# Performance work log

Measured on AMD Instinct MI355X. Metric: run time of the kernel, lower is better.

The kernel has to match this reference:

```python
import jax, jax.numpy as jnp
import numpy as np

H = 512      # hidden_dim
K = 3        # conv_kernel_size
CHUNK = 3    # chunk_size
EPS = 1e-5   # BatchNorm eps


def conv1d(x, w, b, pad):
    # x: (B, Cin, L), w: (Cout, Cin, K)
    y = jax.lax.conv_general_dilated(x, w, (1,), [(pad, pad)],
                                     dimension_numbers=("NCH", "OIH", "NCH"))
    return y + b[None, :, None]


def chunk_indices(seq_lens):
    # static int metadata -> numpy index build (loop over small fixed batch only)
    sl = np.asarray(seq_lens)
    bidx, sidx = [], []
    for b, l in enumerate(sl):
        starts = np.arange(0, int(l) - CHUNK + 1, CHUNK)
        bidx.append(np.full(starts.shape[0], b, dtype=np.int32))
        sidx.append(starts.astype(np.int32))
    return np.concatenate(bidx), np.concatenate(sidx)


def setup_inputs() -> dict:
    key = jax.random.key(0)
    ks = jax.random.split(key, 8)
    B, L = 32, 4096
    x = jax.random.normal(ks[0], (B, L), jnp.float32)
    seq_lens = jax.random.randint(ks[1], (B,), 2048, L + 1)

    def w(k, shape):
        return jax.random.normal(k, shape, jnp.float32) * 0.05

    return {
        "x": x,
        "w0": w(ks[2], (H, 1, K)), "b0": jnp.zeros((H,)), "g0": jnp.ones((H,)), "be0": jnp.zeros((H,)),
        "w1": w(ks[3], (H, H, K)), "b1": jnp.zeros((H,)), "g1": jnp.ones((H,)), "be1": jnp.zeros((H,)),
        "w2": w(ks[4], (H, H, K)), "b2": jnp.zeros((H,)), "g2": jnp.ones((H,)), "be2": jnp.zeros((H,)),
        "pw": w(ks[5], (H, H, CHUNK)), "pb": jnp.zeros((H,)),
        "fw": w(ks[6], (1, H)), "fb": jnp.zeros((1,)),
        "seq_lens": seq_lens,
    }


def reference(x, w0, b0, g0, be0, w1, b1, g1, be1, w2, b2, g2, be2,
              pw, pb, fw, fb, seq_lens):
    inv = np.float32(1.0 / np.sqrt(1.0 + EPS))  # BN eval: mean=0, var=1
    h = x[:, None, :]  # (B, 1, L)
    for (w, b, g, be) in ((w0, b0, g0, be0), (w1, b1, g1, be1), (w2, b2, g2, be2)):
        h = jax.nn.relu(conv1d(h, w, b, pad=1))
        h = (g * inv)[None, :, None] * h + be[None, :, None]
    h = jnp.transpose(h, (0, 2, 1))  # (B, L, H)

    bidx_np, sidx_np = chunk_indices(seq_lens)
    bidx = jnp.asarray(bidx_np)
    sidx = jnp.asarray(sidx_np)
    offs = jnp.arange(CHUNK, dtype=jnp.int32)
    chunks = h[bidx[:, None], sidx[:, None] + offs[None, :], :]  # (N, CHUNK, H)

    # pre_fc_conv over a length-CHUNK window == one GEMM per chunk
    z = jnp.einsum("nth,cht->nc", chunks, pw) + pb  # (N, H)
    logits = jax.nn.relu(z) @ fw.T + fb             # (N, 1)
    return jax.nn.sigmoid(logits)[:, 0]             # (N,)
```

## Files before the change

kernel.cpp:

```cpp
#include <hip/hip_runtime.h>

#define HCH 512
#define LSEQ 4096
#define NB 32
#define KW 3
#define KDIM 1536
#define SPAD 1408
#define INVS 0.9999950000374997f
#define NT 24

typedef __attribute__((ext_vector_type(8))) short bf16x8;
typedef __attribute__((ext_vector_type(4))) float f32x4;

__device__ inline unsigned short f2bf(float f) {
  unsigned int u = __float_as_uint(f);
  u += 0x7fffu + ((u >> 16) & 1u);
  return (unsigned short)(u >> 16);
}

__device__ inline void gl_lds16(const void* g, void* l) {
  __builtin_amdgcn_global_load_lds(
      (const __attribute__((address_space(1))) void*)g,
      (__attribute__((address_space(3))) void*)l, 16, 0, 0);
}

__global__ void prep_all(const float* __restrict__ w1, const float* __restrict__ w2,
                         const float* __restrict__ pw, unsigned short* __restrict__ wt,
                         const int* __restrict__ seq_lens, int* __restrict__ cum,
                         float* __restrict__ pz, int nz) {
  int idx = blockIdx.x * 256 + threadIdx.x;
  if (idx < nz) pz[idx] = 0.f;
  if (idx == 0) {
    int acc = 0;
    for (int b = 0; b < NB; b++) {
      cum[b] = acc;
      acc += (seq_lens[b] - KW) / KW + 1;
    }
  }
  if (idx < 3 * HCH * KDIM) {
    int which = idx / (HCH * KDIM);
    int r = idx % (HCH * KDIM);
    int c = r / KDIM;
    int rem = r % KDIM;
    int k = rem / HCH, ci = rem % HCH;
    const float* src = (which == 0) ? w1 : ((which == 1) ? w2 : pw);
    wt[idx] = f2bf(src[c * KDIM + ci * KW + k]);
  }
}

__global__ void layer0(const float* __restrict__ x, const float* __restrict__ w0,
                       const float* __restrict__ b0, const float* __restrict__ g0,
                       const float* __restrict__ be0, unsigned short* __restrict__ h0,
                       const int* __restrict__ seq_q) {
  int tid = threadIdx.x;
  int wave = tid >> 6, lane = tid & 63;
  int pos0 = (blockIdx.x * 4 + wave) * 8;
  int l0 = pos0 & (LSEQ - 1);
  if (l0 >= seq_q[pos0 >> 12] + 2) return;
  int c0 = lane * 8;

  float w[24], bb[8], gg[8], ee[8];
  for (int v = 0; v < 6; v++)
    *reinterpret_cast<float4*>(w + v * 4) = *reinterpret_cast<const float4*>(w0 + c0 * 3 + v * 4);
  for (int v = 0; v < 2; v++) {
    *reinterpret_cast<float4*>(bb + v * 4) = *reinterpret_cast<const float4*>(b0 + c0 + v * 4);
    *reinterpret_cast<float4*>(gg + v * 4) = *reinterpret_cast<const float4*>(g0 + c0 + v * 4);
    *reinterpret_cast<float4*>(ee + v * 4) = *reinterpret_cast<const float4*>(be0 + c0 + v * 4);
  }
  for (int c = 0; c < 8; c++) gg[c] *= INVS;

  const float* xb = x + (size_t)(pos0 - l0);
  for (int pp = 0; pp < 8; pp++) {
    int l = l0 + pp;
    float xm1 = (l > 0) ? xb[l - 1] : 0.f;
    float xc = xb[l];
    float xp1 = (l < LSEQ - 1) ? xb[l + 1] : 0.f;
    unsigned int o[4];
    for (int pq = 0; pq < 4; pq++) {
      unsigned int lo = 0, hi = 0;
      for (int s = 0; s < 2; s++) {
        int c = pq * 2 + s;
        float y = w[c * 3] * xm1 + w[c * 3 + 1] * xc + w[c * 3 + 2] * xp1 + bb[c];
        y = fmaxf(y, 0.f);
        unsigned int u = f2bf(gg[c] * y + ee[c]);
        if (s == 0) lo = u; else hi = u;
      }
      o[pq] = lo | (hi << 16);
    }
    uint4 v4; v4.x = o[0]; v4.y = o[1]; v4.z = o[2]; v4.w = o[3];
    *reinterpret_cast<uint4*>(h0 + (size_t)(pos0 + pp) * HCH + c0) = v4;
  }
}

#define STAGE_A(Mh, nbuf, tn)                                               \
  { char* d_ = ldsc + ((nbuf)*4 + (Mh)) * 16384 + w * 1024;                 \
    gl_lds16(aSrc[Mh][0] + (tn)*64, d_);                                    \
    gl_lds16(aSrc[Mh][1] + (tn)*64, d_ + 8192); }

#define STAGE_B(Nh, nbuf, tn)                                               \
  { int k_ = (tn) >> 3, ci0_ = ((tn) & 7) << 6;                             \
    int p0_ = bRow[Nh][0] + k_, p1_ = bRow[Nh][1] + k_;                     \
    const unsigned short* s0_ = ((unsigned)p0_ < 4096u)                     \
        ? hin + hb + (size_t)p0_ * HCH + ci0_ + sslot8 : zp + sslot8;       \
    const unsigned short* s1_ = ((unsigned)p1_ < 4096u)                     \
        ? hin + hb + (size_t)p1_ * HCH + ci0_ + sslot8 : zp + sslot8;       \
    char* d_ = ldsc + ((nbuf)*4 + 2 + (Nh)) * 16384 + w * 1024;             \
    gl_lds16(s0_, d_); gl_lds16(s1_, d_ + 8192); }

#define LOAD_AF(Mh, buf)                                                    \
  _Pragma("unroll") for (int i_ = 0; i_ < 4; ++i_)                          \
  _Pragma("unroll") for (int s_ = 0; s_ < 2; ++s_)                          \
    af[i_][s_] = *reinterpret_cast<const bf16x8*>(                          \
        ldsb + ((buf)*4 + (Mh)) * 8192 + (wm + i_*16 + mr) * 64 +           \
        (((s_*4 + quad) ^ (mr & 7)) << 3));

#define LOAD_BF(Nh, buf)                                                    \
  _Pragma("unroll") for (int j_ = 0; j_ < 2; ++j_)                          \
  _Pragma("unroll") for (int s_ = 0; s_ < 2; ++s_)                          \
    bfv[Nh][j_][s_] = *reinterpret_cast<const bf16x8*>(                     \
        ldsb + ((buf)*4 + 2 + (Nh)) * 8192 + (wn + j_*16 + mr) * 64 +       \
        (((s_*4 + quad) ^ (mr & 7)) << 3));

#define MFMA_Q(Mh, Nh)                                                      \
  __builtin_amdgcn_s_setprio(1);                                            \
  _Pragma("unroll") for (int i_ = 0; i_ < 4; ++i_)                          \
  _Pragma("unroll") for (int j_ = 0; j_ < 2; ++j_)                          \
  _Pragma("unroll") for (int s_ = 0; s_ < 2; ++s_)                          \
    acc[(Mh)*4 + i_][(Nh)*2 + j_] = __builtin_amdgcn_mfma_f32_16x16x32_bf16( \
        af[i_][s_], bfv[Nh][j_][s_], acc[(Mh)*4 + i_][(Nh)*2 + j_], 0, 0, 0); \
  __builtin_amdgcn_s_setprio(0);

#define BARRIER { asm volatile("" ::: "memory");                            \
                  __builtin_amdgcn_s_barrier();                             \
                  asm volatile("" ::: "memory"); }
#define WAITV(n) asm volatile("s_waitcnt vmcnt(" #n ")" ::: "memory");

__global__ __launch_bounds__(512, 2) void conv_gemm8(
    const unsigned short* __restrict__ hin,
    const unsigned short* __restrict__ wT,
    const float* __restrict__ bconv, const float* __restrict__ g,
    const float* __restrict__ be,
    unsigned short* __restrict__ hout,
    const unsigned short* __restrict__ zp,
    const int* __restrict__ seq_q, int margin) {
  __shared__ unsigned short ldsb[8 * 8192];

  int f = blockIdx.x;
  int cpx = gridDim.x >> 3;
  int s = (f & 7) * cpx + (f >> 3);
  int cm = (s & 1) << 8;
  int y = s >> 1;
  int b = y >> 4;
  int l0 = (y & 15) << 8;
  int limit = seq_q[b] + margin;
  if (l0 >= limit) return;

  const size_t hb = (size_t)b * LSEQ * HCH;
  int tid = threadIdx.x;
  int w = tid >> 6, lane = tid & 63;
  int quad = lane >> 4, mr = lane & 15;
  int wm = (w >> 2) << 6;
  int wn = (w & 3) << 5;
  int srow = tid >> 3;
  int sslot8 = (((tid & 7) ^ (srow & 7)) << 3);

  const unsigned short* aSrc[2][2];
#pragma unroll
  for (int Mh = 0; Mh < 2; ++Mh)
#pragma unroll
    for (int g2 = 0; g2 < 2; ++g2)
      aSrc[Mh][g2] = wT + (size_t)(cm + Mh*128 + g2*64 + srow) * KDIM + sslot8;
  int bRow[2][2];
#pragma unroll
  for (int Nh = 0; Nh < 2; ++Nh)
#pragma unroll
    for (int g2 = 0; g2 < 2; ++g2)
      bRow[Nh][g2] = l0 - 1 + Nh*128 + g2*64 + srow;

  f32x4 acc[8][4] = {};
  char* ldsc = (char*)ldsb;

  STAGE_A(0, 0, 0); STAGE_A(1, 0, 0); STAGE_B(0, 0, 0); STAGE_B(1, 0, 0);

#pragma unroll 2
  for (int t = 0; t < NT; ++t) {
    int buf = t & 1, nbuf = buf ^ 1;
    int tn = (t + 1 < NT) ? t + 1 : t;
    bf16x8 af[4][2], bfv[2][2][2];
    WAITV(4);
    BARRIER;
    STAGE_A(0, nbuf, tn); STAGE_A(1, nbuf, tn);
    STAGE_B(0, nbuf, tn); STAGE_B(1, nbuf, tn);
    LOAD_AF(0, buf);
    WAITV(8);
    LOAD_BF(0, buf); LOAD_BF(1, buf);
    MFMA_Q(0, 0);
    MFMA_Q(0, 1);
    LOAD_AF(1, buf);
    MFMA_Q(1, 1);
    MFMA_Q(1, 0);
  }

#pragma unroll
  for (int ai = 0; ai < 8; ++ai) {
    int Mh = ai >> 2, i = ai & 3;
    int c = cm + Mh*128 + wm + i*16 + quad*4;
    f32x4 bc = *reinterpret_cast<const f32x4*>(bconv + c);
    f32x4 gg = *reinterpret_cast<const f32x4*>(g + c);
    f32x4 bb = *reinterpret_cast<const f32x4*>(be + c);
#pragma unroll
    for (int aj = 0; aj < 4; ++aj) {
      int Nh = aj >> 1, j = aj & 1;
      int n = l0 + Nh*128 + wn + j*16 + (lane & 15);
      if (n >= limit) continue;
      unsigned long long pack = 0;
#pragma unroll
      for (int r = 0; r < 4; ++r) {
        float yv = acc[ai][aj][r] + bc[r];
        yv = fmaxf(yv, 0.f);
        unsigned long long u = f2bf(gg[r] * INVS * yv + bb[r]);
        pack |= u << (16 * r);
      }
      *reinterpret_cast<unsigned long long*>(hout + hb + (size_t)n * HCH + c) = pack;
    }
  }
}

__global__ __launch_bounds__(256) void chunk_gemm(
    const unsigned short* __restrict__ h2,
    const unsigned short* __restrict__ wTp,
    const float* __restrict__ pb, const float* __restrict__ fw,
    const int* __restrict__ seq_q,
    const int* __restrict__ cum_q,
    float* __restrict__ partial,
    const unsigned short* __restrict__ zp) {
  __shared__ unsigned short As[3 * 128 * 32];
  __shared__ unsigned short Bs[384 * 32];

  int tid = threadIdx.x;
  int wave = tid >> 6, lane = tid & 63;
  int cm = blockIdx.x * 128;
  int b = blockIdx.y / (SPAD / 128);
  int s_base = (blockIdx.y % (SPAD / 128)) * 128;
  int slen = seq_q[b];
  if (3 * s_base + KW > slen) return;
  int p_base = 3 * s_base;
  int wm = (wave >> 1) * 64;
  int wn = (wave & 1) * 64;
  const size_t hb = (size_t)b * LSEQ * HCH;

  f32x4 acc[4][4] = {};

  int lr = lane >> 2, lc = (lane & 3) * 8;

  const unsigned short* bptr[6];
  const unsigned short* aptr[6];
  unsigned aoff[6];
  for (int t = 0; t < 6; t++) {
    int c = wave * 6 + t;
    int p = p_base + c * 16 + lr;
    bptr[t] = (p < LSEQ) ? (h2 + hb + (size_t)p * HCH + lc) : (zp + lc);
    int k = c >> 3, c8 = c & 7;
    aptr[t] = wTp + (size_t)(cm + c8 * 16 + lr) * KDIM + k * HCH + lc;
    aoff[t] = (unsigned)(k * 4096 + c8 * 512) * 2;
  }

  for (int it = 0; it < 16; it++) {
    int ci0 = it * 32;
    for (int t = 0; t < 6; t++) {
      gl_lds16(aptr[t] + ci0, (char*)As + aoff[t]);
      gl_lds16(bptr[t] + ci0, (char*)Bs + (wave * 6 + t) * 1024);
    }
    __syncthreads();

    int quad = lane >> 4, mr = lane & 15;
    for (int t = 0; t < 3; t++) {
      bf16x8 af[4], bfr[4];
      for (int i = 0; i < 4; i++)
        af[i] = *reinterpret_cast<const bf16x8*>(As + t * 4096 + (wm + i * 16 + mr) * 32 + quad * 8);
      for (int j = 0; j < 4; j++)
        bfr[j] = *reinterpret_cast<const bf16x8*>(Bs + (3 * (wn + j * 16 + mr) + t) * 32 + quad * 8);
      for (int i = 0; i < 4; i++)
        for (int j = 0; j < 4; j++)
          acc[i][j] = __builtin_amdgcn_mfma_f32_16x16x32_bf16(af[i], bfr[j], acc[i][j], 0, 0, 0);
    }
    __syncthreads();
  }

  int quad = lane >> 4, nn = lane & 15;
  for (int j = 0; j < 4; j++) {
    float s = 0.f;
    for (int i = 0; i < 4; i++) {
      int c = cm + wm + i * 16 + quad * 4;
      f32x4 pbv = *reinterpret_cast<const f32x4*>(pb + c);
      f32x4 fwv = *reinterpret_cast<const f32x4*>(fw + c);
      for (int r = 0; r < 4; r++) {
        float z = acc[i][j][r] + pbv[r];
        z = fmaxf(z, 0.f);
        s += z * fwv[r];
      }
    }
    s += __shfl_xor(s, 16, 64);
    s += __shfl_xor(s, 32, 64);
    if (quad == 0) {
      int sc = s_base + wn + j * 16 + nn;
      if (3 * sc + KW <= slen) atomicAdd(partial + cum_q[b] + sc, s);
    }
  }
}

__global__ void finalize(const float* __restrict__ partial, const float* __restrict__ fb,
                         float* __restrict__ out, int n) {
  int i = blockIdx.x * 256 + threadIdx.x;
  if (i < n) {
    float t = partial[i] + fb[0];
    out[i] = 1.f / (1.f + expf(-t));
  }
}

extern "C" void kernel_launch(void* const* d_in, const int* in_sizes, int n_in,
                              void* d_out, int out_size, void* d_ws, size_t ws_size,
                              hipStream_t stream) {
  (void)in_sizes; (void)n_in;
  const float* x   = (const float*)d_in[0];
  const float* w0  = (const float*)d_in[1];
  const float* b0  = (const float*)d_in[2];
  const float* g0  = (const float*)d_in[3];
  const float* be0 = (const float*)d_in[4];
  const float* w1  = (const float*)d_in[5];
  const float* b1  = (const float*)d_in[6];
  const float* g1  = (const float*)d_in[7];
  const float* be1 = (const float*)d_in[8];
  const float* w2  = (const float*)d_in[9];
  const float* b2  = (const float*)d_in[10];
  const float* g2  = (const float*)d_in[11];
  const float* be2 = (const float*)d_in[12];
  const float* pw  = (const float*)d_in[13];
  const float* pb  = (const float*)d_in[14];
  const float* fw  = (const float*)d_in[15];
  const float* fb  = (const float*)d_in[16];
  const int* seq_lens = (const int*)d_in[17];

  char* ws = (char*)d_ws;
  unsigned short* zeropage = (unsigned short*)ws;
  float* partial = (float*)(ws + 4096);
  size_t off = 4096 + (size_t)out_size * 4;
  off = (off + 255) & ~(size_t)255;
  int* cum = (int*)(ws + off);
  off += NB * 4;
  off = (off + 255) & ~(size_t)255;
  unsigned short* wt = (unsigned short*)(ws + off);
  off += (size_t)3 * HCH * KDIM * 2;
  off = (off + 255) & ~(size_t)255;
  size_t fixed = off;

  const size_t per_batch = (size_t)LSEQ * HCH * 2;
  int nb_pass = NB;
  while (nb_pass > 1 && fixed + 2 * per_batch * (size_t)nb_pass > ws_size)
    nb_pass >>= 1;
  unsigned short* h0 = (unsigned short*)(ws + fixed);
  unsigned short* h1 = h0 + (size_t)nb_pass * LSEQ * HCH;

  int nzero = 1024 + out_size;
  prep_all<<<(3 * HCH * KDIM) / 256, 256, 0, stream>>>(w1, w2, pw, wt, seq_lens, cum,
                                                       (float*)ws, nzero);

  int npass = NB / nb_pass;
  for (int q = 0; q < npass; q++) {
    const float* xq = x + (size_t)q * nb_pass * LSEQ;
    const int* sq = seq_lens + q * nb_pass;
    int nwg = nb_pass * 32;
    layer0<<<nb_pass * (LSEQ / 32), 256, 0, stream>>>(xq, w0, b0, g0, be0, h0, sq);
    conv_gemm8<<<nwg, 512, 0, stream>>>(h0, wt, b1, g1, be1, h1, zeropage, sq, 1);
    conv_gemm8<<<nwg, 512, 0, stream>>>(h1, wt + (size_t)HCH * KDIM, b2, g2, be2, h0,
                                        zeropage, sq, 0);
    chunk_gemm<<<dim3(4, nb_pass * (SPAD / 128)), 256, 0, stream>>>(
        h0, wt + (size_t)2 * HCH * KDIM, pb, fw,
        sq, cum + q * nb_pass, partial, zeropage);
  }
  finalize<<<(out_size + 255) / 256, 256, 0, stream>>>(partial, fb, (float*)d_out, out_size);
}
```

Baseline: 614.4 us.

## Pad activation buffers with zero rows and deepen B prefetch pipeline in conv GEMM

Activation buffers get a zeroed halo row on each side of every sequence (stride LSEQ+4), which removes the per-load bounds check and zero-page redirection for the conv B operand. The conv GEMM main loop is fully unrolled into 24 steps with A double-buffered and B triple-buffered, so B loads are issued two steps ahead. The K loop order is also changed to interleave the three taps. LDS use rises to 160KB per block, which may limit occupancy to one block per CU despite launch_bounds(512,2).

```diff
diff --git a/kernel.cpp b/kernel.cpp
--- a/kernel.cpp
+++ b/kernel.cpp
@@ -2,6 +2,7 @@
 
 #define HCH 512
 #define LSEQ 4096
+#define HSTR (LSEQ + 4)
 #define NB 32
 #define KW 3
 #define KDIM 1536
@@ -27,7 +28,8 @@
 __global__ void prep_all(const float* __restrict__ w1, const float* __restrict__ w2,
                          const float* __restrict__ pw, unsigned short* __restrict__ wt,
                          const int* __restrict__ seq_lens, int* __restrict__ cum,
-                         float* __restrict__ pz, int nz) {
+                         float* __restrict__ pz, int nz,
+                         unsigned short* __restrict__ hbuf, int nbp) {
   int idx = blockIdx.x * 256 + threadIdx.x;
   if (idx < nz) pz[idx] = 0.f;
   if (idx == 0) {
@@ -36,6 +38,15 @@
       cum[b] = acc;
       acc += (seq_lens[b] - KW) / KW + 1;
     }
+  }
+  int npads = 2 * nbp * 4 * HCH;
+  if (idx < npads) {
+    int per = nbp * 4 * HCH;
+    int buf = idx / per, r = idx % per;
+    int b = r / (4 * HCH), rr = r % (4 * HCH);
+    int j = rr / HCH, c = rr % HCH;
+    int row = (j == 0) ? 0 : (LSEQ + j);
+    hbuf[((size_t)buf * nbp + b) * HSTR * HCH + (size_t)row * HCH + c] = 0;
   }
   if (idx < 3 * HCH * KDIM) {
     int which = idx / (HCH * KDIM);
@@ -56,7 +67,8 @@
   int wave = tid >> 6, lane = tid & 63;
   int pos0 = (blockIdx.x * 4 + wave) * 8;
   int l0 = pos0 & (LSEQ - 1);
-  if (l0 >= seq_q[pos0 >> 12] + 2) return;
+  int bq = pos0 >> 12;
+  if (l0 >= seq_q[bq] + 2) return;
   int c0 = lane * 8;
 
   float w[24], bb[8], gg[8], ee[8];
@@ -70,6 +82,7 @@
   for (int c = 0; c < 8; c++) gg[c] *= INVS;
 
   const float* xb = x + (size_t)(pos0 - l0);
+  unsigned short* hrow = h0 + ((size_t)bq * HSTR + 1 + l0) * HCH + c0;
   for (int pp = 0; pp < 8; pp++) {
     int l = l0 + pp;
     float xm1 = (l > 0) ? xb[l - 1] : 0.f;
@@ -88,38 +101,35 @@
       o[pq] = lo | (hi << 16);
     }
     uint4 v4; v4.x = o[0]; v4.y = o[1]; v4.z = o[2]; v4.w = o[3];
-    *reinterpret_cast<uint4*>(h0 + (size_t)(pos0 + pp) * HCH + c0) = v4;
-  }
-}
-
-#define STAGE_A(Mh, nbuf, tn)                                               \
-  { char* d_ = ldsc + ((nbuf)*4 + (Mh)) * 16384 + w * 1024;                 \
-    gl_lds16(aSrc[Mh][0] + (tn)*64, d_);                                    \
-    gl_lds16(aSrc[Mh][1] + (tn)*64, d_ + 8192); }
-
-#define STAGE_B(Nh, nbuf, tn)                                               \
-  { int k_ = (tn) >> 3, ci0_ = ((tn) & 7) << 6;                             \
-    int p0_ = bRow[Nh][0] + k_, p1_ = bRow[Nh][1] + k_;                     \
-    const unsigned short* s0_ = ((unsigned)p0_ < 4096u)                     \
-        ? hin + hb + (size_t)p0_ * HCH + ci0_ + sslot8 : zp + sslot8;       \
-    const unsigned short* s1_ = ((unsigned)p1_ < 4096u)                     \
-        ? hin + hb + (size_t)p1_ * HCH + ci0_ + sslot8 : zp + sslot8;       \
-    char* d_ = ldsc + ((nbuf)*4 + 2 + (Nh)) * 16384 + w * 1024;             \
-    gl_lds16(s0_, d_); gl_lds16(s1_, d_ + 8192); }
-
-#define LOAD_AF(Mh, buf)                                                    \
+    *reinterpret_cast<uint4*>(hrow + (size_t)pp * HCH) = v4;
+  }
+}
+
+#define OFFK(T) (((T) % 3) * HCH + ((T) / 3) * 64)
+
+#define STAGE_A(Mh, AB, TN)                                                 \
+  { char* d_ = ldsc + (AB) * 32768 + (Mh) * 16384 + w * 1024;               \
+    gl_lds16(aSrc[Mh][0] + OFFK(TN), d_);                                   \
+    gl_lds16(aSrc[Mh][1] + OFFK(TN), d_ + 8192); }
+
+#define STAGE_B(Nh, BB, TN)                                                 \
+  { char* d_ = ldsc + 65536 + (BB) * 32768 + (Nh) * 16384 + w * 1024;       \
+    gl_lds16(bSrc[Nh][0] + OFFK(TN), d_);                                   \
+    gl_lds16(bSrc[Nh][1] + OFFK(TN), d_ + 8192); }
+
+#define LOAD_AF(Mh, AB)                                                     \
   _Pragma("unroll") for (int i_ = 0; i_ < 4; ++i_)                          \
   _Pragma("unroll") for (int s_ = 0; s_ < 2; ++s_)                          \
     af[i_][s_] = *reinterpret_cast<const bf16x8*>(                          \
-        ldsb + ((buf)*4 + (Mh)) * 8192 + (wm + i_*16 + mr) * 64 +           \
-        (((s_*4 + quad) ^ (mr & 7)) << 3));
-
-#define LOAD_BF(Nh, buf)                                                    \
+        ldsb + (AB) * 16384 + (Mh) * 8192 + (wm + i_ * 16 + mr) * 64 +      \
+        (((s_ * 4 + quad) ^ (mr & 7)) << 3));
+
+#define LOAD_BF(Nh, BB)                                                     \
   _Pragma("unroll") for (int j_ = 0; j_ < 2; ++j_)                          \
   _Pragma("unroll") for (int s_ = 0; s_ < 2; ++s_)                          \
     bfv[Nh][j_][s_] = *reinterpret_cast<const bf16x8*>(                     \
-        ldsb + ((buf)*4 + 2 + (Nh)) * 8192 + (wn + j_*16 + mr) * 64 +       \
-        (((s_*4 + quad) ^ (mr & 7)) << 3));
+        ldsb + 32768 + (BB) * 16384 + (Nh) * 8192 + (wn + j_ * 16 + mr) * 64 + \
+        (((s_ * 4 + quad) ^ (mr & 7)) << 3));
 
 #define MFMA_Q(Mh, Nh)                                                      \
   __builtin_amdgcn_s_setprio(1);                                            \
@@ -135,15 +145,30 @@
                   asm volatile("" ::: "memory"); }
 #define WAITV(n) asm volatile("s_waitcnt vmcnt(" #n ")" ::: "memory");
 
+#define STEP(T)                                                             \
+  {                                                                         \
+    if ((T) == NT - 1) { WAITV(0); } else { WAITV(4); }                     \
+    BARRIER;                                                                \
+    if ((T) + 1 < NT) { STAGE_A(0, ((T)+1)&1, (T)+1);                       \
+                        STAGE_A(1, ((T)+1)&1, (T)+1); }                     \
+    if ((T) + 2 < NT) { STAGE_B(0, ((T)+2)%3, (T)+2);                       \
+                        STAGE_B(1, ((T)+2)%3, (T)+2); }                     \
+    bf16x8 af[4][2], bfv[2][2][2];                                          \
+    LOAD_AF(0, (T)&1);                                                      \
+    LOAD_BF(0, (T)%3); LOAD_BF(1, (T)%3);                                   \
+    MFMA_Q(0, 0); MFMA_Q(0, 1);                                             \
+    LOAD_AF(1, (T)&1);                                                      \
+    MFMA_Q(1, 1); MFMA_Q(1, 0);                                             \
+  }
+
 __global__ __launch_bounds__(512, 2) void conv_gemm8(
     const unsigned short* __restrict__ hin,
     const unsigned short* __restrict__ wT,
     const float* __restrict__ bconv, const float* __restrict__ g,
     const float* __restrict__ be,
     unsigned short* __restrict__ hout,
-    const unsigned short* __restrict__ zp,
     const int* __restrict__ seq_q, int margin) {
-  __shared__ unsigned short ldsb[8 * 8192];
+  __shared__ unsigned short ldsb[81920];
 
   int f = blockIdx.x;
   int cpx = gridDim.x >> 3;
@@ -155,7 +180,7 @@
   int limit = seq_q[b] + margin;
   if (l0 >= limit) return;
 
-  const size_t hb = (size_t)b * LSEQ * HCH;
+  const size_t hb = (size_t)b * HSTR * HCH + HCH;
   int tid = threadIdx.x;
   int w = tid >> 6, lane = tid & 63;
   int quad = lane >> 4, mr = lane & 15;
@@ -169,49 +194,38 @@
   for (int Mh = 0; Mh < 2; ++Mh)
 #pragma unroll
     for (int g2 = 0; g2 < 2; ++g2)
-      aSrc[Mh][g2] = wT + (size_t)(cm + Mh*128 + g2*64 + srow) * KDIM + sslot8;
-  int bRow[2][2];
+      aSrc[Mh][g2] = wT + (size_t)(cm + Mh * 128 + g2 * 64 + srow) * KDIM + sslot8;
+  const unsigned short* bSrc[2][2];
 #pragma unroll
   for (int Nh = 0; Nh < 2; ++Nh)
 #pragma unroll
     for (int g2 = 0; g2 < 2; ++g2)
-      bRow[Nh][g2] = l0 - 1 + Nh*128 + g2*64 + srow;
+      bSrc[Nh][g2] = hin + hb +
+          (size_t)(l0 - 1 + Nh * 128 + g2 * 64 + srow) * HCH + sslot8;
 
   f32x4 acc[8][4] = {};
   char* ldsc = (char*)ldsb;
 
-  STAGE_A(0, 0, 0); STAGE_A(1, 0, 0); STAGE_B(0, 0, 0); STAGE_B(1, 0, 0);
-
-#pragma unroll 2
-  for (int t = 0; t < NT; ++t) {
-    int buf = t & 1, nbuf = buf ^ 1;
-    int tn = (t + 1 < NT) ? t + 1 : t;
-    bf16x8 af[4][2], bfv[2][2][2];
-    WAITV(4);
-    BARRIER;
-    STAGE_A(0, nbuf, tn); STAGE_A(1, nbuf, tn);
-    STAGE_B(0, nbuf, tn); STAGE_B(1, nbuf, tn);
-    LOAD_AF(0, buf);
-    WAITV(8);
-    LOAD_BF(0, buf); LOAD_BF(1, buf);
-    MFMA_Q(0, 0);
-    MFMA_Q(0, 1);
-    LOAD_AF(1, buf);
-    MFMA_Q(1, 1);
-    MFMA_Q(1, 0);
-  }
+  STAGE_A(0, 0, 0); STAGE_A(1, 0, 0);
+  STAGE_B(0, 0, 0); STAGE_B(1, 0, 0);
+  STAGE_B(0, 1, 1); STAGE_B(1, 1, 1);
+
+  STEP(0)  STEP(1)  STEP(2)  STEP(3)  STEP(4)  STEP(5)
+  STEP(6)  STEP(7)  STEP(8)  STEP(9)  STEP(10) STEP(11)
+  STEP(12) STEP(13) STEP(14) STEP(15) STEP(16) STEP(17)
+  STEP(18) STEP(19) STEP(20) STEP(21) STEP(22) STEP(23)
 
 #pragma unroll
   for (int ai = 0; ai < 8; ++ai) {
     int Mh = ai >> 2, i = ai & 3;
-    int c = cm + Mh*128 + wm + i*16 + quad*4;
+    int c = cm + Mh * 128 + wm + i * 16 + quad * 4;
     f32x4 bc = *reinterpret_cast<const f32x4*>(bconv + c);
     f32x4 gg = *reinterpret_cast<const f32x4*>(g + c);
     f32x4 bb = *reinterpret_cast<const f32x4*>(be + c);
 #pragma unroll
     for (int aj = 0; aj < 4; ++aj) {
       int Nh = aj >> 1, j = aj & 1;
-      int n = l0 + Nh*128 + wn + j*16 + (lane & 15);
+      int n = l0 + Nh * 128 + wn + j * 16 + (lane & 15);
       if (n >= limit) continue;
       unsigned long long pack = 0;
 #pragma unroll
@@ -247,7 +261,7 @@
   int p_base = 3 * s_base;
   int wm = (wave >> 1) * 64;
   int wn = (wave & 1) * 64;
-  const size_t hb = (size_t)b * LSEQ * HCH;
+  const size_t hb = (size_t)b * HSTR * HCH + HCH;
 
   f32x4 acc[4][4] = {};
 
@@ -354,16 +368,16 @@
   off = (off + 255) & ~(size_t)255;
   size_t fixed = off;
 
-  const size_t per_batch = (size_t)LSEQ * HCH * 2;
+  const size_t per_batch = (size_t)HSTR * HCH * 2;
   int nb_pass = NB;
   while (nb_pass > 1 && fixed + 2 * per_batch * (size_t)nb_pass > ws_size)
     nb_pass >>= 1;
   unsigned short* h0 = (unsigned short*)(ws + fixed);
-  unsigned short* h1 = h0 + (size_t)nb_pass * LSEQ * HCH;
+  unsigned short* h1 = h0 + (size_t)nb_pass * HSTR * HCH;
 
   int nzero = 1024 + out_size;
   prep_all<<<(3 * HCH * KDIM) / 256, 256, 0, stream>>>(w1, w2, pw, wt, seq_lens, cum,
-                                                       (float*)ws, nzero);
+                                                       (float*)ws, nzero, h0, nb_pass);
 
   int npass = NB / nb_pass;
   for (int q = 0; q < npass; q++) {
@@ -371,9 +385,9 @@
     const int* sq = seq_lens + q * nb_pass;
     int nwg = nb_pass * 32;
     layer0<<<nb_pass * (LSEQ / 32), 256, 0, stream>>>(xq, w0, b0, g0, be0, h0, sq);
-    conv_gemm8<<<nwg, 512, 0, stream>>>(h0, wt, b1, g1, be1, h1, zeropage, sq, 1);
+    conv_gemm8<<<nwg, 512, 0, stream>>>(h0, wt, b1, g1, be1, h1, sq, 1);
     conv_gemm8<<<nwg, 512, 0, stream>>>(h1, wt + (size_t)HCH * KDIM, b2, g2, be2, h0,
-                                        zeropage, sq, 0);
+                                        sq, 0);
     chunk_gemm<<<dim3(4, nb_pass * (SPAD / 128)), 256, 0, stream>>>(
         h0, wt + (size_t)2 * HCH * KDIM, pb, fw,
         sq, cum + q * nb_pass, partial, zeropage);
```

New measurement: 599.4 us. 1.03x faster.
